# Optimization experiments

Hardware: AMD Instinct MI355X
Metric: run time of the kernel (lower is better)

Reference implementation:

```python
import jax, jax.numpy as jnp
import numpy as np

D_MODEL = 1024
H = 16
D_HEAD = D_MODEL // H
MASK_VAL = -1e30


def setup_inputs() -> dict:
    key = jax.random.key(0)
    ks = jax.random.split(key, 10)
    B, S = 2, 2048
    scale = 1.0 / np.sqrt(D_MODEL)
    return {
        "query": jax.random.normal(ks[0], (B, S, D_MODEL), jnp.float32),
        "key": jax.random.normal(ks[1], (B, S, D_MODEL), jnp.float32),
        "value": jax.random.normal(ks[2], (B, S, D_MODEL), jnp.float32),
        "mask": jax.random.randint(ks[3], (B, S, S), 0, 2) > 0,
        "Wq": jax.random.normal(ks[4], (D_MODEL, D_MODEL), jnp.float32) * scale,
        "bq": jnp.zeros((D_MODEL,), jnp.float32),
        "Wk": jax.random.normal(ks[5], (D_MODEL, D_MODEL), jnp.float32) * scale,
        "bk": jnp.zeros((D_MODEL,), jnp.float32),
        "Wv": jax.random.normal(ks[6], (D_MODEL, D_MODEL), jnp.float32) * scale,
        "bv": jnp.zeros((D_MODEL,), jnp.float32),
    }


def _split_heads(x, B, S):
    # [B,S,D] -> [B,H,S,Dh]
    return x.reshape(B, S, H, D_HEAD).transpose(0, 2, 1, 3)


def reference(query, key, value, mask, Wq, bq, Wk, bk, Wv, bv):
    B, S, _ = query.shape
    q = _split_heads(query @ Wq.T + bq, B, S)
    k = _split_heads(key @ Wk.T + bk, B, S)
    v = _split_heads(value @ Wv.T + bv, B, S)
    # scale by sqrt of per-head dim (query.size(-1) after split)
    q = q / jnp.sqrt(jnp.asarray(D_HEAD, q.dtype))
    scores = jnp.einsum("bhqd,bhkd->bhqk", q, k)
    scores = jnp.where(mask[:, None, :, :], MASK_VAL, scores)
    attn = jax.nn.softmax(scores, axis=-1)
    out = jnp.einsum("bhqk,bhkd->bhqd", attn, v)
    return out.transpose(0, 2, 1, 3).reshape(B, S, D_MODEL)
```

## Files before the change

### kernel.cpp

```cpp
#include <hip/hip_runtime.h>
#include <hip/hip_bf16.h>

#define D_MODEL 1024
#define NH 16
#define DH 64
#define S_LEN 2048
#define BATCH 2
#define NEG_BIG -3e38f
#define QSCALE (0.125f * 1.44269504088896f)

#define KV_HSTRIDE (S_LEN * DH)
#define WS_V_OFF   (NH * KV_HSTRIDE)
#define KVB_WORDS  (2 * NH * KV_HSTRIDE)
#define MB_WORDS   ((S_LEN / 64) * S_LEN)
#define KTILE 128
#define NT (S_LEN / KTILE)
#define X_ELEMS (BATCH * S_LEN * D_MODEL)
#define W_ELEMS (D_MODEL * D_MODEL)

typedef __attribute__((ext_vector_type(8))) short bf16x8;
typedef __attribute__((ext_vector_type(4))) float f32x4;

static __device__ inline unsigned short f2bf(float f) {
    union { float f; unsigned u; } v; v.f = f;
    unsigned r = v.u + 0x7fffu + ((v.u >> 16) & 1u);
    return (unsigned short)(r >> 16);
}
static __device__ inline unsigned cvt2(float a, float b) {
    union { __hip_bfloat162 h2; unsigned u; } cv;
    cv.h2 = __float22bfloat162_rn(make_float2(a, b));
    return cv.u;
}
static __device__ inline bf16x8 pack8(f32x4 a, f32x4 b) {
    union { bf16x8 v; unsigned u[4]; } r;
    r.u[0] = cvt2(a[0], a[1]); r.u[1] = cvt2(a[2], a[3]);
    r.u[2] = cvt2(b[0], b[1]); r.u[3] = cvt2(b[2], b[3]);
    return r.v;
}
static __device__ inline bf16x8 cvt8(const float* __restrict__ p) {
    return pack8(*(const f32x4*)p, *(const f32x4*)(p + 4));
}
static __device__ inline float exp2_fast(float x) {
#if __has_builtin(__builtin_amdgcn_exp2f)
    return __builtin_amdgcn_exp2f(x);
#else
    return exp2f(x);
#endif
}
static __device__ inline void gload_lds16(const unsigned short* __restrict__ g,
                                          unsigned short* l, int lane) {
#if __has_builtin(__builtin_amdgcn_global_load_lds)
    __builtin_amdgcn_global_load_lds(
        (const __attribute__((address_space(1))) void*)g,
        (__attribute__((address_space(3))) void*)l, 16, 0, 0);
#else
    *(bf16x8*)((char*)l + lane * 16) = *(const bf16x8*)g;
#endif
}
static __device__ inline int vperm(int s) {
    return (s & ~31) | ((s & 15) << 1) | ((s >> 4) & 1);
}

__global__ __launch_bounds__(256) void cvt_kernel(
    const float* __restrict__ q, const float* __restrict__ k,
    const float* __restrict__ v,
    const float* __restrict__ Wq, const float* __restrict__ Wk,
    const float* __restrict__ Wv,
    unsigned short* __restrict__ xb, unsigned short* __restrict__ wb)
{
    const int by = blockIdx.y;
    const float* src;
    unsigned short* dst;
    int t;
    if (blockIdx.x < 1024) {
        src = by == 0 ? q : (by == 1 ? k : v);
        dst = xb + (size_t)by * X_ELEMS;
        t = blockIdx.x * 256 + threadIdx.x;
    } else {
        src = by == 0 ? Wq : (by == 1 ? Wk : Wv);
        dst = wb + (size_t)by * W_ELEMS;
        t = (blockIdx.x - 1024) * 256 + threadIdx.x;
    }
    const size_t o = (size_t)t * 16;
    *(bf16x8*)&dst[o]     = cvt8(src + o);
    *(bf16x8*)&dst[o + 8] = cvt8(src + o + 8);
}

__global__ __launch_bounds__(256) void pack_mask_kernel(
    const int* __restrict__ mask, unsigned long long* __restrict__ mbits,
    int b_base)
{
    const int w    = blockIdx.x * 4 + (threadIdx.x >> 6);
    const int lane = threadIdx.x & 63;
    const int b    = b_base + (w >> 16);
    const int rem  = w & 65535;
    const int kt   = rem >> 11;
    const int s    = rem & 2047;
    const int v = mask[((size_t)b * S_LEN + s) * S_LEN + kt * 64 + lane];
    const unsigned long long bits = __ballot(v != 0);
    if (lane == 0) mbits[w] = bits;
}

__global__ __launch_bounds__(256) void proj_v2_kernel(
    const unsigned short* __restrict__ xb, const unsigned short* __restrict__ wb,
    const float* __restrict__ bq, const float* __restrict__ bk,
    const float* __restrict__ bv,
    float* __restrict__ q_out, unsigned short* __restrict__ ws)
{
    const int bx = blockIdx.x;
    const int by = blockIdx.y;
    const int z  = by >> 3;
    const int c0 = (by & 7) * 128;

    const unsigned short* A  = xb + (size_t)z * X_ELEMS;
    const unsigned short* Bw = wb + (size_t)z * W_ELEMS;
    const float* bias = z == 0 ? bq : (z == 1 ? bk : bv);

    const int tid  = threadIdx.x;
    const int wave = tid >> 6;
    const int lane = tid & 63;
    const int quad = lane >> 4;
    const int l16  = lane & 15;
    const int m0   = (wave & 1) * 64;
    const int n0   = (wave >> 1) * 64;

    __shared__ __align__(16) unsigned short As[128 * 32];
    __shared__ __align__(16) unsigned short Bs[128 * 32];

    const int r_lo = wave * 16 + (lane >> 2);
    const int r_hi = (wave + 4) * 16 + (lane >> 2);
    const int segu = (lane & 3) * 8;
    const int row0 = bx * 128;

    f32x4 acc[4][4] = {};

    for (int kk = 0; kk < D_MODEL; kk += 32) {
        gload_lds16(A  + (size_t)(row0 + r_lo) * D_MODEL + kk + segu, &As[wave * 512], lane);
        gload_lds16(A  + (size_t)(row0 + r_hi) * D_MODEL + kk + segu, &As[(wave + 4) * 512], lane);
        gload_lds16(Bw + (size_t)(c0 + r_lo) * D_MODEL + kk + segu, &Bs[wave * 512], lane);
        gload_lds16(Bw + (size_t)(c0 + r_hi) * D_MODEL + kk + segu, &Bs[(wave + 4) * 512], lane);
        __syncthreads();

        bf16x8 af[4], bfr[4];
#pragma unroll
        for (int i = 0; i < 4; ++i)
            af[i] = *(const bf16x8*)&As[(m0 + i * 16 + l16) * 32 + quad * 8];
#pragma unroll
        for (int j = 0; j < 4; ++j)
            bfr[j] = *(const bf16x8*)&Bs[(n0 + j * 16 + l16) * 32 + quad * 8];
#pragma unroll
        for (int i = 0; i < 4; ++i)
#pragma unroll
            for (int j = 0; j < 4; ++j)
                acc[i][j] = __builtin_amdgcn_mfma_f32_16x16x32_bf16(
                    af[i], bfr[j], acc[i][j], 0, 0, 0);
        __syncthreads();
    }

#pragma unroll
    for (int j = 0; j < 4; ++j) {
        const int cl  = c0 + n0 + j * 16 + l16;
        const float bval = bias[cl];
        const int h  = cl >> 6;
        const int dh = cl & 63;
#pragma unroll
        for (int i = 0; i < 4; ++i) {
#pragma unroll
            for (int r = 0; r < 4; ++r) {
                const int row = row0 + m0 + i * 16 + quad * 4 + r;
                const float v = acc[i][j][r] + bval;
                if (z == 0) {
                    q_out[(size_t)row * D_MODEL + cl] = v * QSCALE;
                } else {
                    unsigned short* slab = ws + (size_t)(row >> 11) * KVB_WORDS;
                    const int s = row & 2047;
                    if (z == 1)
                        slab[(size_t)h * KV_HSTRIDE + s * DH + dh] = f2bf(v);
                    else
                        slab[WS_V_OFF + (size_t)h * KV_HSTRIDE + dh * S_LEN + vperm(s)] = f2bf(v);
                }
            }
        }
    }
}

__global__ __launch_bounds__(256) void proj_fb_kernel(
    const float* __restrict__ q_in, const float* __restrict__ k_in,
    const float* __restrict__ v_in,
    const float* __restrict__ Wq, const float* __restrict__ bq,
    const float* __restrict__ Wk, const float* __restrict__ bk,
    const float* __restrict__ Wv, const float* __restrict__ bv,
    float* __restrict__ q_out, unsigned short* __restrict__ ws, int b_base)
{
    const int bx = blockIdx.x;
    const int by = blockIdx.y;
    const int z  = by >> 3;
    const int c0 = (by & 7) * 128;

    const float* x    = z == 0 ? q_in : (z == 1 ? k_in : v_in);
    const float* W    = z == 0 ? Wq   : (z == 1 ? Wk   : Wv);
    const float* bias = z == 0 ? bq   : (z == 1 ? bk   : bv);

    const int tid  = threadIdx.x;
    const int wave = tid >> 6;
    const int lane = tid & 63;
    const int quad = lane >> 4;
    const int l16  = lane & 15;
    const int m0   = (wave & 1) * 64;
    const int n0   = (wave >> 1) * 64;

    __shared__ __align__(16) unsigned short As[128][40];
    __shared__ __align__(16) unsigned short Bs[128][40];

    const int srow = tid >> 1;
    const int kcol = (tid & 1) * 16;
    const int row0 = b_base * S_LEN + bx * 128;
    const float* ag = x + (size_t)(row0 + srow) * D_MODEL + kcol;
    const float* bg = W + (size_t)(c0 + srow) * D_MODEL + kcol;

    f32x4 acc[4][4] = {};

    for (int kk = 0; kk < D_MODEL; kk += 32) {
        {
            f32x4 a0 = *(const f32x4*)(ag + kk);
            f32x4 a1 = *(const f32x4*)(ag + kk + 4);
            f32x4 a2 = *(const f32x4*)(ag + kk + 8);
            f32x4 a3 = *(const f32x4*)(ag + kk + 12);
            f32x4 b0 = *(const f32x4*)(bg + kk);
            f32x4 b1 = *(const f32x4*)(bg + kk + 4);
            f32x4 b2 = *(const f32x4*)(bg + kk + 8);
            f32x4 b3 = *(const f32x4*)(bg + kk + 12);
            *(bf16x8*)&As[srow][kcol]     = pack8(a0, a1);
            *(bf16x8*)&As[srow][kcol + 8] = pack8(a2, a3);
            *(bf16x8*)&Bs[srow][kcol]     = pack8(b0, b1);
            *(bf16x8*)&Bs[srow][kcol + 8] = pack8(b2, b3);
        }
        __syncthreads();

        bf16x8 af[4], bfr[4];
#pragma unroll
        for (int i = 0; i < 4; ++i)
            af[i] = *(const bf16x8*)&As[m0 + i * 16 + l16][quad * 8];
#pragma unroll
        for (int j = 0; j < 4; ++j)
            bfr[j] = *(const bf16x8*)&Bs[n0 + j * 16 + l16][quad * 8];
#pragma unroll
        for (int i = 0; i < 4; ++i)
#pragma unroll
            for (int j = 0; j < 4; ++j)
                acc[i][j] = __builtin_amdgcn_mfma_f32_16x16x32_bf16(
                    af[i], bfr[j], acc[i][j], 0, 0, 0);
        __syncthreads();
    }

#pragma unroll
    for (int j = 0; j < 4; ++j) {
        const int cl  = c0 + n0 + j * 16 + l16;
        const float bval = bias[cl];
        const int h  = cl >> 6;
        const int dh = cl & 63;
#pragma unroll
        for (int i = 0; i < 4; ++i) {
#pragma unroll
            for (int r = 0; r < 4; ++r) {
                const int row = row0 + m0 + i * 16 + quad * 4 + r;
                const float v = acc[i][j][r] + bval;
                if (z == 0) {
                    q_out[(size_t)row * D_MODEL + cl] = v * QSCALE;
                } else {
                    const int b_rel = (row >> 11) - b_base;
                    const int s     = row & 2047;
                    unsigned short* slab = ws + (size_t)b_rel * KVB_WORDS;
                    if (z == 1)
                        slab[(size_t)h * KV_HSTRIDE + s * DH + dh] = f2bf(v);
                    else
                        slab[WS_V_OFF + (size_t)h * KV_HSTRIDE + dh * S_LEN + vperm(s)] = f2bf(v);
                }
            }
        }
    }
}

__global__ __launch_bounds__(256) void attn_kernel(
    const unsigned short* __restrict__ ws,
    const unsigned long long* __restrict__ mbits,
    const int* __restrict__ mask,
    float* __restrict__ out, int b_base, int use_bits)
{
    const int h     = blockIdx.x;
    const int qtile = blockIdx.y;
    const int bz    = blockIdx.z;
    const int b0    = b_base + bz;

    const unsigned short* K  = ws + (size_t)bz * KVB_WORDS + (size_t)h * KV_HSTRIDE;
    const unsigned short* Vg = K + WS_V_OFF;
    const unsigned long long* mb = mbits + (size_t)bz * MB_WORDS;

    const int tid  = threadIdx.x;
    const int wave = tid >> 6;
    const int lane = tid & 63;
    const int quad = lane >> 4;
    const int l16  = lane & 15;
    const int q0   = qtile * 64;

    __shared__ __align__(16) unsigned short Vt[64][136];
    __shared__ __align__(16) unsigned short KP[128 * 72];

    bf16x8 aq0, aq1;
    {
        const float* qrow =
            out + (size_t)(b0 * S_LEN + q0 + wave * 16 + l16) * D_MODEL + h * DH;
        aq0 = cvt8(qrow + quad * 8);
        aq1 = cvt8(qrow + 32 + quad * 8);
    }

    float l_r[4] = {0.f, 0.f, 0.f, 0.f};
    f32x4 o_acc[4] = {};

    const int qg_base = q0 + wave * 16 + quad * 4;
    const int mask_row0 = (b0 * S_LEN + qg_base) * S_LEN;

    const int krow = tid >> 1, kc = (tid & 1) * 32;
    const int vrow = tid >> 2, vc = (tid & 3) * 32;
    bf16x8 kr[4], vr[4];
    {
        const unsigned short* kp = K + (size_t)krow * DH + kc;
        const unsigned short* vp = Vg + (size_t)vrow * S_LEN + vc;
#pragma unroll
        for (int i = 0; i < 4; ++i) {
            kr[i] = *(const bf16x8*)(kp + 8 * i);
            vr[i] = *(const bf16x8*)(vp + 8 * i);
        }
    }

    for (int kt = 0; kt < NT; ++kt) {
#pragma unroll
        for (int i = 0; i < 4; ++i) {
            *(bf16x8*)&KP[krow * 72 + kc + 8 * i] = kr[i];
            *(bf16x8*)&Vt[vrow][vc + 8 * i]       = vr[i];
        }
        __syncthreads();

        if (kt + 1 < NT) {
            const unsigned short* kp = K + (size_t)((kt + 1) * KTILE + krow) * DH + kc;
            const unsigned short* vp = Vg + (size_t)vrow * S_LEN + (kt + 1) * KTILE + vc;
#pragma unroll
            for (int i = 0; i < 4; ++i) {
                kr[i] = *(const bf16x8*)(kp + 8 * i);
                vr[i] = *(const bf16x8*)(vp + 8 * i);
            }
        }
        unsigned long long wm0[4], wm1[4];
        if (use_bits) {
#pragma unroll
            for (int r = 0; r < 4; ++r) {
                wm0[r] = mb[(2 * kt) * S_LEN + qg_base + r];
                wm1[r] = mb[(2 * kt + 1) * S_LEN + qg_base + r];
            }
        }

        f32x4 s[8];
#pragma unroll
        for (int blk = 0; blk < 8; ++blk) {
            const unsigned short* kb = &KP[(blk * 16 + l16) * 72];
            bf16x8 bk0 = *(const bf16x8*)&kb[quad * 8];
            bf16x8 bk1 = *(const bf16x8*)&kb[32 + quad * 8];
            s[blk] = (f32x4){0.f, 0.f, 0.f, 0.f};
            s[blk] = __builtin_amdgcn_mfma_f32_16x16x32_bf16(aq0, bk0, s[blk], 0, 0, 0);
            s[blk] = __builtin_amdgcn_mfma_f32_16x16x32_bf16(aq1, bk1, s[blk], 0, 0, 0);
        }

#pragma unroll
        for (int r = 0; r < 4; ++r) {
            float sum = 0.0f;
            if (use_bits) {
#pragma unroll
                for (int blk = 0; blk < 8; ++blk) {
                    const unsigned long long w = (blk < 4) ? wm0[r] : wm1[r];
                    const unsigned half = (unsigned)(w >> (((blk >> 1) & 1) * 32));
                    const bool masked = (half >> (((blk & 1) << 4) + l16)) & 1u;
                    const float p = masked ? 0.0f : exp2_fast(s[blk][r]);
                    s[blk][r] = p;
                    sum += p;
                }
            } else {
#pragma unroll
                for (int blk = 0; blk < 8; ++blk) {
                    const int kg = kt * KTILE + blk * 16 + l16;
                    const float p = mask[mask_row0 + r * S_LEN + kg]
                                        ? 0.0f : exp2_fast(s[blk][r]);
                    s[blk][r] = p;
                    sum += p;
                }
            }
            sum += __shfl_xor(sum, 1, 64);
            sum += __shfl_xor(sum, 2, 64);
            sum += __shfl_xor(sum, 4, 64);
            sum += __shfl_xor(sum, 8, 64);
            l_r[r] += sum;
        }

        __syncthreads();

        unsigned* Pt32 = (unsigned*)&KP[wave * (16 * 136)];
#pragma unroll
        for (int bp = 0; bp < 4; ++bp)
#pragma unroll
            for (int r = 0; r < 4; ++r)
                Pt32[(quad * 4 + r) * 68 + bp * 16 + l16] =
                    cvt2(s[2 * bp][r], s[2 * bp + 1][r]);

        const unsigned short* Pt = &KP[wave * (16 * 136)];
        bf16x8 ap[4];
#pragma unroll
        for (int j = 0; j < 4; ++j)
            ap[j] = *(const bf16x8*)&Pt[l16 * 136 + j * 32 + quad * 8];

#pragma unroll
        for (int d = 0; d < 4; ++d) {
#pragma unroll
            for (int j = 0; j < 4; ++j) {
                bf16x8 bv = *(const bf16x8*)&Vt[d * 16 + l16][j * 32 + quad * 8];
                o_acc[d] = __builtin_amdgcn_mfma_f32_16x16x32_bf16(ap[j], bv, o_acc[d], 0, 0, 0);
            }
        }
        __syncthreads();
    }

#pragma unroll
    for (int r = 0; r < 4; ++r) {
        const float inv = 1.0f / fmaxf(l_r[r], 1e-30f);
        const int qg = qg_base + r;
#pragma unroll
        for (int d = 0; d < 4; ++d)
            out[((size_t)(b0 * S_LEN) + qg) * D_MODEL + h * DH + d * 16 + l16] =
                o_acc[d][r] * inv;
    }
}

extern "C" void kernel_launch(void* const* d_in, const int* in_sizes, int n_in,
                              void* d_out, int out_size, void* d_ws, size_t ws_size,
                              hipStream_t stream) {
    const float* query = (const float*)d_in[0];
    const float* key   = (const float*)d_in[1];
    const float* value = (const float*)d_in[2];
    const int*   mask  = (const int*)d_in[3];
    const float* Wq    = (const float*)d_in[4];
    const float* bq    = (const float*)d_in[5];
    const float* Wk    = (const float*)d_in[6];
    const float* bk    = (const float*)d_in[7];
    const float* Wv    = (const float*)d_in[8];
    const float* bv    = (const float*)d_in[9];

    unsigned short* ws   = (unsigned short*)d_ws;
    float*          outp = (float*)d_out;

    const size_t KV_BYTES = (size_t)KVB_WORDS * 2;
    const size_t MB_BYTES = (size_t)MB_WORDS * 8;
    const size_t XB_BYTES = (size_t)3 * X_ELEMS * 2;
    const size_t WB_BYTES = (size_t)3 * W_ELEMS * 2;
    const size_t base2    = 2 * KV_BYTES + 2 * MB_BYTES;

    if (ws_size >= base2 + XB_BYTES + WB_BYTES) {
        unsigned long long* mbits = (unsigned long long*)(ws + 2 * KVB_WORDS);
        unsigned short* xb = ws + base2 / 2;
        unsigned short* wb = xb + (size_t)3 * X_ELEMS;
        cvt_kernel<<<dim3(1280, 3), 256, 0, stream>>>(
            query, key, value, Wq, Wk, Wv, xb, wb);
        proj_v2_kernel<<<dim3(32, 24), 256, 0, stream>>>(
            xb, wb, bq, bk, bv, outp, ws);
        pack_mask_kernel<<<dim3(2 * MB_WORDS / 4), 256, 0, stream>>>(mask, mbits, 0);
        attn_kernel<<<dim3(NH, S_LEN / 64, 2), 256, 0, stream>>>(
            ws, mbits, mask, outp, 0, 1);
    } else if (ws_size >= base2) {
        unsigned long long* mbits = (unsigned long long*)(ws + 2 * KVB_WORDS);
        proj_fb_kernel<<<dim3(32, 24), 256, 0, stream>>>(
            query, key, value, Wq, bq, Wk, bk, Wv, bv, outp, ws, 0);
        pack_mask_kernel<<<dim3(2 * MB_WORDS / 4), 256, 0, stream>>>(mask, mbits, 0);
        attn_kernel<<<dim3(NH, S_LEN / 64, 2), 256, 0, stream>>>(
            ws, mbits, mask, outp, 0, 1);
    } else if (ws_size >= KV_BYTES + MB_BYTES) {
        unsigned long long* mbits = (unsigned long long*)(ws + KVB_WORDS);
        for (int b0 = 0; b0 < BATCH; ++b0) {
            proj_fb_kernel<<<dim3(16, 24), 256, 0, stream>>>(
                query, key, value, Wq, bq, Wk, bk, Wv, bv, outp, ws, b0);
            pack_mask_kernel<<<dim3(MB_WORDS / 4), 256, 0, stream>>>(mask, mbits, b0);
            attn_kernel<<<dim3(NH, S_LEN / 64, 1), 256, 0, stream>>>(
                ws, mbits, mask, outp, b0, 1);
        }
    } else {
        for (int b0 = 0; b0 < BATCH; ++b0) {
            proj_fb_kernel<<<dim3(16, 24), 256, 0, stream>>>(
                query, key, value, Wq, bq, Wk, bk, Wv, bv, outp, ws, b0);
            attn_kernel<<<dim3(NH, S_LEN / 64, 1), 256, 0, stream>>>(
                ws, (const unsigned long long*)ws, mask, outp, b0, 0);
        }
    }
}
```

Before: 284.1 us.

## Compute transposed scores so P stays in registers as the PV MFMA operand

Swaps the MFMA operand order to compute S^T (keys along rows), so each lane's exp'd probabilities can be packed directly into the A operand of the P·V MFMA instead of round-tripping through LDS. This removes the P LDS write and read and one __syncthreads per tile, and defers row-sum reduction to the end. The V permutation (vperm) and mask bit layout are changed to match the new key ordering, and the K LDS stride is changed to 88 to alter bank conflicts. The design relies on the V layout and mask packing elsewhere being consistent with the new permutation.

```diff
diff --git a/kernel.cpp b/kernel.cpp
--- a/kernel.cpp
+++ b/kernel.cpp
@@ -17,6 +17,7 @@
 #define NT (S_LEN / KTILE)
 #define X_ELEMS (BATCH * S_LEN * D_MODEL)
 #define W_ELEMS (D_MODEL * D_MODEL)
+#define KSTR 88
 
 typedef __attribute__((ext_vector_type(8))) short bf16x8;
 typedef __attribute__((ext_vector_type(4))) float f32x4;
@@ -58,7 +59,7 @@
 #endif
 }
 static __device__ inline int vperm(int s) {
-    return (s & ~31) | ((s & 15) << 1) | ((s >> 4) & 1);
+    return (s & ~31) | ((s & 12) << 1) | ((s & 16) >> 2) | (s & 3);
 }
 
 __global__ __launch_bounds__(256) void cvt_kernel(
@@ -304,7 +305,7 @@
     const int q0   = qtile * 64;
 
     __shared__ __align__(16) unsigned short Vt[64][136];
-    __shared__ __align__(16) unsigned short KP[128 * 72];
+    __shared__ __align__(16) unsigned short Kt[128 * KSTR];
 
     bf16x8 aq0, aq1;
     {
@@ -314,11 +315,9 @@
         aq1 = cvt8(qrow + 32 + quad * 8);
     }
 
-    float l_r[4] = {0.f, 0.f, 0.f, 0.f};
+    const int qg = q0 + wave * 16 + l16;
+    float l_lane = 0.f;
     f32x4 o_acc[4] = {};
-
-    const int qg_base = q0 + wave * 16 + quad * 4;
-    const int mask_row0 = (b0 * S_LEN + qg_base) * S_LEN;
 
     const int krow = tid >> 1, kc = (tid & 1) * 32;
     const int vrow = tid >> 2, vc = (tid & 3) * 32;
@@ -336,8 +335,8 @@
     for (int kt = 0; kt < NT; ++kt) {
 #pragma unroll
         for (int i = 0; i < 4; ++i) {
-            *(bf16x8*)&KP[krow * 72 + kc + 8 * i] = kr[i];
-            *(bf16x8*)&Vt[vrow][vc + 8 * i]       = vr[i];
+            *(bf16x8*)&Kt[krow * KSTR + kc + 8 * i] = kr[i];
+            *(bf16x8*)&Vt[vrow][vc + 8 * i]         = vr[i];
         }
         __syncthreads();
 
@@ -350,90 +349,76 @@
                 vr[i] = *(const bf16x8*)(vp + 8 * i);
             }
         }
-        unsigned long long wm0[4], wm1[4];
+
+        unsigned long long wm0 = 0ull, wm1 = 0ull;
         if (use_bits) {
+            wm0 = mb[(size_t)(2 * kt) * S_LEN + qg] >> (quad * 4);
+            wm1 = mb[(size_t)(2 * kt + 1) * S_LEN + qg] >> (quad * 4);
+        }
+
+        f32x4 s[8];
+#pragma unroll
+        for (int blk = 0; blk < 8; ++blk) {
+            const unsigned short* kb = &Kt[(blk * 16 + l16) * KSTR];
+            bf16x8 k0 = *(const bf16x8*)&kb[quad * 8];
+            bf16x8 k1 = *(const bf16x8*)&kb[32 + quad * 8];
+            s[blk] = (f32x4){0.f, 0.f, 0.f, 0.f};
+            s[blk] = __builtin_amdgcn_mfma_f32_16x16x32_bf16(k0, aq0, s[blk], 0, 0, 0);
+            s[blk] = __builtin_amdgcn_mfma_f32_16x16x32_bf16(k1, aq1, s[blk], 0, 0, 0);
+        }
+
+#pragma unroll
+        for (int blk = 0; blk < 8; ++blk) {
+            const unsigned long long w = (blk < 4) ? wm0 : wm1;
+            const int sh = (blk & 3) * 16;
 #pragma unroll
             for (int r = 0; r < 4; ++r) {
-                wm0[r] = mb[(2 * kt) * S_LEN + qg_base + r];
-                wm1[r] = mb[(2 * kt + 1) * S_LEN + qg_base + r];
+                bool masked;
+                if (use_bits) {
+                    masked = (w >> (sh + r)) & 1ull;
+                } else {
+                    const int kg = kt * KTILE + blk * 16 + quad * 4 + r;
+                    masked = mask[((size_t)(b0 * S_LEN) + qg) * S_LEN + kg] != 0;
+                }
+                const float p = masked ? 0.0f : exp2_fast(s[blk][r]);
+                s[blk][r] = p;
+                l_lane += p;
             }
         }
 
-        f32x4 s[8];
-#pragma unroll
-        for (int blk = 0; blk < 8; ++blk) {
-            const unsigned short* kb = &KP[(blk * 16 + l16) * 72];
-            bf16x8 bk0 = *(const bf16x8*)&kb[quad * 8];
-            bf16x8 bk1 = *(const bf16x8*)&kb[32 + quad * 8];
-            s[blk] = (f32x4){0.f, 0.f, 0.f, 0.f};
-            s[blk] = __builtin_amdgcn_mfma_f32_16x16x32_bf16(aq0, bk0, s[blk], 0, 0, 0);
-            s[blk] = __builtin_amdgcn_mfma_f32_16x16x32_bf16(aq1, bk1, s[blk], 0, 0, 0);
-        }
-
-#pragma unroll
-        for (int r = 0; r < 4; ++r) {
-            float sum = 0.0f;
-            if (use_bits) {
-#pragma unroll
-                for (int blk = 0; blk < 8; ++blk) {
-                    const unsigned long long w = (blk < 4) ? wm0[r] : wm1[r];
-                    const unsigned half = (unsigned)(w >> (((blk >> 1) & 1) * 32));
-                    const bool masked = (half >> (((blk & 1) << 4) + l16)) & 1u;
-                    const float p = masked ? 0.0f : exp2_fast(s[blk][r]);
-                    s[blk][r] = p;
-                    sum += p;
-                }
-            } else {
-#pragma unroll
-                for (int blk = 0; blk < 8; ++blk) {
-                    const int kg = kt * KTILE + blk * 16 + l16;
-                    const float p = mask[mask_row0 + r * S_LEN + kg]
-                                        ? 0.0f : exp2_fast(s[blk][r]);
-                    s[blk][r] = p;
-                    sum += p;
-                }
+        bf16x8 af[4];
+#pragma unroll
+        for (int c = 0; c < 4; ++c) {
+            union { bf16x8 v; unsigned u[4]; } pk;
+            pk.u[0] = cvt2(s[2 * c][0],     s[2 * c][1]);
+            pk.u[1] = cvt2(s[2 * c][2],     s[2 * c][3]);
+            pk.u[2] = cvt2(s[2 * c + 1][0], s[2 * c + 1][1]);
+            pk.u[3] = cvt2(s[2 * c + 1][2], s[2 * c + 1][3]);
+            af[c] = pk.v;
+        }
+
+#pragma unroll
+        for (int d = 0; d < 4; ++d) {
+#pragma unroll
+            for (int c = 0; c < 4; ++c) {
+                bf16x8 bv = *(const bf16x8*)&Vt[d * 16 + l16][c * 32 + quad * 8];
+                o_acc[d] = __builtin_amdgcn_mfma_f32_16x16x32_bf16(af[c], bv, o_acc[d], 0, 0, 0);
             }
-            sum += __shfl_xor(sum, 1, 64);
-            sum += __shfl_xor(sum, 2, 64);
-            sum += __shfl_xor(sum, 4, 64);
-            sum += __shfl_xor(sum, 8, 64);
-            l_r[r] += sum;
-        }
-
-        __syncthreads();
-
-        unsigned* Pt32 = (unsigned*)&KP[wave * (16 * 136)];
-#pragma unroll
-        for (int bp = 0; bp < 4; ++bp)
-#pragma unroll
-            for (int r = 0; r < 4; ++r)
-                Pt32[(quad * 4 + r) * 68 + bp * 16 + l16] =
-                    cvt2(s[2 * bp][r], s[2 * bp + 1][r]);
-
-        const unsigned short* Pt = &KP[wave * (16 * 136)];
-        bf16x8 ap[4];
-#pragma unroll
-        for (int j = 0; j < 4; ++j)
-            ap[j] = *(const bf16x8*)&Pt[l16 * 136 + j * 32 + quad * 8];
-
-#pragma unroll
-        for (int d = 0; d < 4; ++d) {
-#pragma unroll
-            for (int j = 0; j < 4; ++j) {
-                bf16x8 bv = *(const bf16x8*)&Vt[d * 16 + l16][j * 32 + quad * 8];
-                o_acc[d] = __builtin_amdgcn_mfma_f32_16x16x32_bf16(ap[j], bv, o_acc[d], 0, 0, 0);
-            }
-        }
-        __syncthreads();
-    }
+        }
+        __syncthreads();
+    }
+
+    l_lane += __shfl_xor(l_lane, 16, 64);
+    l_lane += __shfl_xor(l_lane, 32, 64);
 
 #pragma unroll
     for (int r = 0; r < 4; ++r) {
-        const float inv = 1.0f / fmaxf(l_r[r], 1e-30f);
-        const int qg = qg_base + r;
+        const float lsum = __shfl(l_lane, quad * 4 + r, 64);
+        const float inv  = 1.0f / fmaxf(lsum, 1e-30f);
+        const int qgr = q0 + wave * 16 + quad * 4 + r;
 #pragma unroll
         for (int d = 0; d < 4; ++d)
-            out[((size_t)(b0 * S_LEN) + qg) * D_MODEL + h * DH + d * 16 + l16] =
+            out[((size_t)(b0 * S_LEN) + qgr) * D_MODEL + h * DH + d * 16 + l16] =
                 o_acc[d][r] * inv;
     }
 }
```

New measurement: 274.4 us. -3.4%, faster.
